# Kernel tuning notes

Hardware: AMD Instinct MI355X
Metric: run time of the kernel (lower is better)

Reference implementation:

```python
import jax, jax.numpy as jnp
import numpy as np

B, S = 1, 2048
H = 1024          # hidden_size
HQ = 16           # num_attention_heads
HKV = 1           # num_key_value_heads (MQA; required for torch matmul broadcast)
D = H // HQ       # head_dim = 64
FF = 4096         # intermediate_size
V = 32000         # vocab_size
L = 2             # num_hidden_layers
EPS = 1e-6


def setup_inputs() -> dict:
    key = jax.random.key(0)
    ks = jax.random.split(key, 12)
    s = 0.02
    return {
        "input_ids": jax.random.randint(ks[0], (B, S), 0, V, dtype=jnp.int32),
        "embed": jax.random.normal(ks[1], (V, H), jnp.float32) * s,
        "Wq": jax.random.normal(ks[2], (L, H, H), jnp.float32) * s,
        "Wk": jax.random.normal(ks[3], (L, HKV * D, H), jnp.float32) * s,
        "Wv": jax.random.normal(ks[4], (L, HKV * D, H), jnp.float32) * s,
        "Wo": jax.random.normal(ks[5], (L, H, H), jnp.float32) * s,
        "Wg": jax.random.normal(ks[6], (L, FF, H), jnp.float32) * s,
        "Wu": jax.random.normal(ks[7], (L, FF, H), jnp.float32) * s,
        "Wd": jax.random.normal(ks[8], (L, H, FF), jnp.float32) * s,
        "ln1": jnp.ones((L, H), jnp.float32),
        "ln2": jnp.ones((L, H), jnp.float32),
    }


def _rmsnorm(x, w):
    return x * jax.lax.rsqrt(jnp.mean(x * x, axis=-1, keepdims=True) + EPS) * w


def _rope(x):
    # x: [B, h, S, D]; module hardcodes base 10000 (ignores config theta)
    d = x.shape[-1]
    inv = 1.0 / (10000.0 ** (jnp.arange(0, d, 2, dtype=jnp.float32) / d))  # [d/2]
    freqs = jnp.arange(x.shape[2], dtype=jnp.float32)[:, None] * inv       # [S, d/2]
    cos, sin = jnp.cos(freqs), jnp.sin(freqs)
    x1, x2 = x[..., : d // 2], x[..., d // 2 :]
    return jnp.concatenate([x1 * cos - x2 * sin, x2 * cos + x1 * sin], axis=-1)


def _forward(input_ids, embed, Wq, Wk, Wv, Wo, Wg, Wu, Wd, ln1, ln2):
    x = embed[input_ids]  # [B, S, H]
    scale = 1.0 / jnp.sqrt(jnp.float32(D))
    for l in range(L):
        # --- attention ---
        h = _rmsnorm(x, ln1[l])
        q = (h @ Wq[l].T).reshape(B, S, HQ, D).transpose(0, 2, 1, 3)   # [B,HQ,S,D]
        k = (h @ Wk[l].T).reshape(B, S, HKV, D).transpose(0, 2, 1, 3)  # [B,1,S,D]
        v = (h @ Wv[l].T).reshape(B, S, HKV, D).transpose(0, 2, 1, 3)
        q, k = _rope(q), _rope(k)
        kk, vv = k[:, 0], v[:, 0]                                      # [B,S,D] (MQA broadcast)
        scores = jnp.einsum("bhqd,bkd->bhqk", q, kk) * scale           # [B,HQ,S,S] (no causal mask!)
        attn = jax.nn.softmax(scores, axis=-1)
        o = jnp.einsum("bhqk,bkd->bhqd", attn, vv)                     # [B,HQ,S,D]
        o = o.transpose(0, 2, 1, 3).reshape(B, S, H) @ Wo[l].T
        x = x + o
        # --- mlp (SwiGLU) ---
        h = _rmsnorm(x, ln2[l])
        x = x + (jax.nn.silu(h @ Wg[l].T) * (h @ Wu[l].T)) @ Wd[l].T
    return x


def reference(input_ids, embed, Wq, Wk, Wv, Wo, Wg, Wu, Wd, ln1, ln2):
    return _forward(input_ids, embed, Wq, Wk, Wv, Wo, Wg, Wu, Wd, ln1, ln2)
```

## Files before the change

kernel.cpp:

```cpp
#include <hip/hip_runtime.h>
#include <math.h>

#define S_LEN 2048
#define H_DIM 1024
#define NHQ 16
#define D_HEAD 64
#define FF_DIM 4096
#define NLAYER 2
#define EPSV 1e-6f
#define QKV_N 1152

typedef unsigned short ushortt;
typedef __attribute__((ext_vector_type(8))) short bf16x8;
typedef __attribute__((ext_vector_type(4))) short bf16x4;
typedef __attribute__((ext_vector_type(4))) float f32x4;
typedef __attribute__((ext_vector_type(16))) float f32x16;

__device__ __forceinline__ float bf2f(ushortt u) {
    union { float f; unsigned u; } c; c.u = ((unsigned)u) << 16; return c.f;
}
__device__ __forceinline__ ushortt f2bf(float f) {
    union { float f; unsigned u; } c; c.f = f;
    unsigned r = c.u + 0x7fff + ((c.u >> 16) & 1);
    return (ushortt)(r >> 16);
}
__device__ __forceinline__ unsigned cvtpk(float a, float b) {
    unsigned r;
    asm("v_cvt_pk_bf16_f32 %0, %1, %2" : "=v"(r) : "v"(a), "v"(b));
    return r;
}
__device__ __forceinline__ bf16x8 mk8(unsigned a, unsigned b, unsigned c, unsigned d) {
    union { unsigned u[4]; bf16x8 v; } t; t.u[0] = a; t.u[1] = b; t.u[2] = c; t.u[3] = d; return t.v;
}

__device__ __forceinline__ void gload_lds16(const ushortt* g, ushortt* l) {
    __builtin_amdgcn_global_load_lds(
        (const __attribute__((address_space(1))) unsigned int*)g,
        (__attribute__((address_space(3))) unsigned int*)l, 16, 0, 0);
}

__global__ __launch_bounds__(256) void f2b_k(const float* __restrict__ in,
                                             ushortt* __restrict__ out, long n) {
    long i8 = ((long)blockIdx.x * 256 + threadIdx.x) * 8;
    if (i8 >= n) return;
    f32x4 a = *(const f32x4*)&in[i8];
    f32x4 b = *(const f32x4*)&in[i8 + 4];
    bf16x8 o;
    #pragma unroll
    for (int j = 0; j < 4; j++) { o[j] = (short)f2bf(a[j]); o[4 + j] = (short)f2bf(b[j]); }
    *(bf16x8*)&out[i8] = o;
}

__global__ __launch_bounds__(256) void gather_k(const int* __restrict__ ids,
                                                const float* __restrict__ emb,
                                                float* __restrict__ x) {
    int row = blockIdx.x, tid = threadIdx.x;
    long id = ids[row];
    f32x4 e = *((const f32x4*)emb + id * (H_DIM / 4) + tid);
    *(f32x4*)&x[(long)row * H_DIM + tid * 4] = e;
}

__global__ __launch_bounds__(256) void rmsnorm_k(const float* __restrict__ x,
                                                 const float* __restrict__ w,
                                                 ushortt* __restrict__ out) {
    __shared__ float red[4];
    int row = blockIdx.x, tid = threadIdx.x;
    f32x4 v = *(const f32x4*)&x[(long)row * H_DIM + tid * 4];
    float ss = v[0]*v[0] + v[1]*v[1] + v[2]*v[2] + v[3]*v[3];
    #pragma unroll
    for (int off = 1; off < 64; off <<= 1) ss += __shfl_xor(ss, off, 64);
    if ((tid & 63) == 0) red[tid >> 6] = ss;
    __syncthreads();
    float tot = red[0] + red[1] + red[2] + red[3];
    float rs = rsqrtf(tot / (float)H_DIM + EPSV);
    f32x4 wv = *(const f32x4*)&w[tid * 4];
    #pragma unroll
    for (int j = 0; j < 4; j++)
        out[(long)row * H_DIM + tid * 4 + j] = f2bf(v[j] * rs * wv[j]);
}

template <int EPI>
__global__ __launch_bounds__(256) void gemm64(const ushortt* __restrict__ A,
                                              const ushortt* __restrict__ B,
                                              void* __restrict__ out,
                                              int M, int N, int K, int lda) {
    __shared__ ushortt As[2][64 * 64];
    __shared__ ushortt Bs[2][64 * 64];
    const int tid = threadIdx.x;
    const int lane = tid & 63;
    const int w = tid >> 6;
    const int wm = w >> 1, wn = w & 1;
    const int m0 = blockIdx.y * 64, n0 = blockIdx.x * 64;
    const int r15 = lane & 15, g = lane >> 4;

    const int sr = tid >> 3;
    const int scel = (tid & 7) * 8;
    const int swz = ((sr & 7) << 3);
    const int srcel = scel ^ swz;

    const ushortt* pa0 = &A[(long)(m0 + sr) * lda + srcel];
    const ushortt* pa1 = &A[(long)(m0 + 32 + sr) * lda + srcel];
    const ushortt* pb0 = &B[(long)(n0 + sr) * K + srcel];
    const ushortt* pb1 = &B[(long)(n0 + 32 + sr) * K + srcel];
    const int l0 = sr * 64 + scel, l1 = (32 + sr) * 64 + scel;

    f32x4 acc[2][2] = {};

#define STAGE(buf, t)                              \
    do {                                           \
        int kk_ = (t) * 64;                        \
        gload_lds16(pa0 + kk_, &As[buf][l0]);      \
        gload_lds16(pa1 + kk_, &As[buf][l1]);      \
        gload_lds16(pb0 + kk_, &Bs[buf][l0]);      \
        gload_lds16(pb1 + kk_, &Bs[buf][l1]);      \
    } while (0)

    STAGE(0, 0);
    asm volatile("s_waitcnt vmcnt(0)" : : : "memory");
    __builtin_amdgcn_s_barrier();

    const int NT = K / 64;
    int cur = 0;
    for (int t = 0; t < NT; ++t) {
        if (t + 1 < NT) STAGE(cur ^ 1, t + 1);

        bf16x8 a[2][2], b[2][2];
        #pragma unroll
        for (int mf = 0; mf < 2; mf++)
            #pragma unroll
            for (int ks = 0; ks < 2; ks++) {
                int row = wm * 32 + mf * 16 + r15;
                a[mf][ks] = *(bf16x8*)&As[cur][row * 64 + ((ks * 32 + g * 8) ^ ((row & 7) << 3))];
            }
        #pragma unroll
        for (int nf = 0; nf < 2; nf++)
            #pragma unroll
            for (int ks = 0; ks < 2; ks++) {
                int row = wn * 32 + nf * 16 + r15;
                b[nf][ks] = *(bf16x8*)&Bs[cur][row * 64 + ((ks * 32 + g * 8) ^ ((row & 7) << 3))];
            }
        #pragma unroll
        for (int ks = 0; ks < 2; ks++)
            #pragma unroll
            for (int mf = 0; mf < 2; mf++)
                #pragma unroll
                for (int nf = 0; nf < 2; nf++)
                    acc[mf][nf] = __builtin_amdgcn_mfma_f32_16x16x32_bf16(
                        a[mf][ks], b[nf][ks], acc[mf][nf], 0, 0, 0);

        asm volatile("s_waitcnt vmcnt(0)" : : : "memory");
        __builtin_amdgcn_s_barrier();
        cur ^= 1;
    }
#undef STAGE

    #pragma unroll
    for (int mf = 0; mf < 2; mf++)
        #pragma unroll
        for (int nf = 0; nf < 2; nf++)
            #pragma unroll
            for (int r = 0; r < 4; r++) {
                int row = m0 + wm * 32 + mf * 16 + g * 4 + r;
                int col = n0 + wn * 32 + nf * 16 + r15;
                float v = acc[mf][nf][r];
                if (EPI == 0) ((ushortt*)out)[(long)row * N + col] = f2bf(v);
                else ((float*)out)[(long)row * N + col] += v;
            }
}

__global__ __launch_bounds__(256) void rope_k(const ushortt* __restrict__ src,
                                              ushortt* __restrict__ dst,
                                              int nheads, int sstride, int dstride) {
    int idx = blockIdx.x * 256 + threadIdx.x;
    int total = S_LEN * nheads * 32;
    if (idx >= total) return;
    int i = idx & 31;
    int hd = (idx >> 5) % nheads;
    int s = idx / (32 * nheads);
    long sb = (long)s * sstride + hd * 64 + i;
    long db = (long)s * dstride + hd * 64 + i;
    float x1 = bf2f(src[sb]), x2 = bf2f(src[sb + 32]);
    float inv = expf(-((2.f * i) / 64.f) * 9.210340371976184f);
    float f = (float)s * inv;
    float sn, cs;
    sincosf(f, &sn, &cs);
    dst[db] = f2bf(x1 * cs - x2 * sn);
    dst[db + 32] = f2bf(x2 * cs + x1 * sn);
}

__global__ __launch_bounds__(256) void vtr_k(const ushortt* __restrict__ qkv,
                                             ushortt* __restrict__ vt) {
    __shared__ ushortt t[64][66];
    int s0 = blockIdx.x * 64;
    int grp = threadIdx.x >> 6, lane = threadIdx.x & 63;
    #pragma unroll
    for (int i = 0; i < 16; i++) {
        int r = grp * 16 + i;
        t[r][lane] = qkv[(long)(s0 + r) * QKV_N + NHQ * D_HEAD + D_HEAD + lane];
    }
    __syncthreads();
    #pragma unroll
    for (int i = 0; i < 16; i++) {
        int d = grp * 16 + i;
        vt[(long)d * S_LEN + s0 + lane] = t[lane][d];
    }
}

__device__ __forceinline__ void attn_body32(const bf16x8 ka[4], const bf16x8 va[4],
                                            const bf16x8 bq[4],
                                            f32x16& O0, f32x16& O1,
                                            float& lrun, int hb) {
    f32x16 s = {};
    #pragma unroll
    for (int ds = 0; ds < 4; ds++)
        s = __builtin_amdgcn_mfma_f32_32x32x16_bf16(ka[ds], bq[ds], s, 0, 0, 0);

    float p[16];
    float ps = 0.f;
    #pragma unroll
    for (int i = 0; i < 16; i++) {
        p[i] = __expf(s[i] * 0.125f);
        ps += p[i];
    }
    lrun += ps;

    unsigned w[8], x[8];
    #pragma unroll
    for (int t = 0; t < 8; t++) w[t] = cvtpk(p[2 * t], p[2 * t + 1]);
    #pragma unroll
    for (int t = 0; t < 8; t++) x[t] = __shfl_xor(w[t], 32, 64);
    bf16x8 B0 = hb ? mk8(x[2], x[3], w[2], w[3]) : mk8(w[0], w[1], x[0], x[1]);
    bf16x8 B1 = hb ? mk8(x[6], x[7], w[6], w[7]) : mk8(w[4], w[5], x[4], x[5]);

    O0 = __builtin_amdgcn_mfma_f32_32x32x16_bf16(va[0], B0, O0, 0, 0, 0);
    O0 = __builtin_amdgcn_mfma_f32_32x32x16_bf16(va[1], B1, O0, 0, 0, 0);
    O1 = __builtin_amdgcn_mfma_f32_32x32x16_bf16(va[2], B0, O1, 0, 0, 0);
    O1 = __builtin_amdgcn_mfma_f32_32x32x16_bf16(va[3], B1, O1, 0, 0, 0);
}

__global__ __launch_bounds__(256) void attn4_k(const ushortt* __restrict__ qkv,
                                               const ushortt* __restrict__ kb,
                                               const ushortt* __restrict__ vt,
                                               ushortt* __restrict__ o) {
    __shared__ float Olds[4][32 * 68];
    __shared__ float Llds[4][32];
    const int tid = threadIdx.x;
    const int w = tid >> 6;
    const int lane = tid & 63;
    const int l31 = lane & 31, hb = lane >> 5;
    const int h = blockIdx.y;
    const int q0 = blockIdx.x * 32;

    bf16x8 bq[4];
    #pragma unroll
    for (int ds = 0; ds < 4; ds++)
        bq[ds] = *(const bf16x8*)&qkv[(long)(q0 + l31) * QKV_N + h * D_HEAD + ds * 16 + hb * 8];

#define LOADKV(KA, VA, J0)                                                                \
    do {                                                                                  \
        _Pragma("unroll") for (int ds = 0; ds < 4; ds++)                                  \
            KA[ds] = *(const bf16x8*)&kb[(long)((J0) + l31) * D_HEAD + ds * 16 + hb * 8]; \
        _Pragma("unroll") for (int t = 0; t < 4; t++)                                     \
            VA[t] = *(const bf16x8*)&vt[(long)((t >> 1) * 32 + l31) * S_LEN + (J0) +      \
                                        (t & 1) * 16 + hb * 8];                           \
    } while (0)

    f32x16 O0 = {}, O1 = {};
    float lrun = 0.f;

    const int jbeg = w * (S_LEN / 4);
    const int jend = jbeg + (S_LEN / 4);

    bf16x8 kaA[4], vaA[4], kaB[4], vaB[4];
    LOADKV(kaA, vaA, jbeg);
    for (int j0 = jbeg; j0 < jend; j0 += 64) {
        LOADKV(kaB, vaB, j0 + 32);
        attn_body32(kaA, vaA, bq, O0, O1, lrun, hb);
        if (j0 + 64 < jend) LOADKV(kaA, vaA, j0 + 64);
        attn_body32(kaB, vaB, bq, O0, O1, lrun, hb);
    }
#undef LOADKV

    float ltot = lrun + __shfl_xor(lrun, 32, 64);
    #pragma unroll
    for (int r = 0; r < 16; r++) {
        int d = (r & 3) + 8 * (r >> 2) + 4 * hb;
        Olds[w][l31 * 68 + d] = O0[r];
        Olds[w][l31 * 68 + 32 + d] = O1[r];
    }
    if (hb == 0) Llds[w][l31] = ltot;
    __syncthreads();

    const int q = tid >> 3, d0 = (tid & 7) * 8;
    float denom = Llds[0][q] + Llds[1][q] + Llds[2][q] + Llds[3][q];
    float inv = 1.f / denom;
    float acc[8] = {};
    #pragma unroll
    for (int z = 0; z < 4; z++) {
        const float* p = &Olds[z][q * 68 + d0];
        f32x4 a = *(const f32x4*)p;
        f32x4 b = *(const f32x4*)(p + 4);
        #pragma unroll
        for (int j = 0; j < 4; j++) { acc[j] += a[j]; acc[4 + j] += b[j]; }
    }
    bf16x8 ov;
    #pragma unroll
    for (int j = 0; j < 8; j++) ov[j] = (short)f2bf(acc[j] * inv);
    *(bf16x8*)&o[(long)(q0 + q) * H_DIM + h * D_HEAD + d0] = ov;
}

__global__ __launch_bounds__(256) void silu_mul_k(const ushortt* __restrict__ gub,
                                                  ushortt* __restrict__ out, int n) {
    int idx = blockIdx.x * 256 + threadIdx.x;
    if (idx >= n) return;
    int row = idx >> 12;
    int c = idx & (FF_DIM - 1);
    float a = bf2f(gub[(long)row * (2 * FF_DIM) + c]);
    float b = bf2f(gub[(long)row * (2 * FF_DIM) + FF_DIM + c]);
    float r = (a / (1.f + __expf(-a))) * b;
    out[(long)row * (2 * FF_DIM) + c] = f2bf(r);
}

__global__ __launch_bounds__(256) void copy_out_k(const float* __restrict__ x,
                                                  float* __restrict__ out, int n4) {
    int idx = blockIdx.x * 256 + threadIdx.x;
    if (idx >= n4) return;
    *(f32x4*)&out[(long)idx * 4] = *(const f32x4*)&x[(long)idx * 4];
}

extern "C" void kernel_launch(void* const* d_in, const int* in_sizes, int n_in,
                              void* d_out, int out_size, void* d_ws, size_t ws_size,
                              hipStream_t stream) {
    const int* ids = (const int*)d_in[0];
    const float* emb = (const float*)d_in[1];
    const float* Wq = (const float*)d_in[2];
    const float* Wk = (const float*)d_in[3];
    const float* Wv = (const float*)d_in[4];
    const float* Wo = (const float*)d_in[5];
    const float* Wg = (const float*)d_in[6];
    const float* Wu = (const float*)d_in[7];
    const float* Wd = (const float*)d_in[8];
    const float* ln1 = (const float*)d_in[9];
    const float* ln2 = (const float*)d_in[10];

    char* ws = (char*)d_ws;
    float* x = (float*)ws;        ws += (size_t)S_LEN * H_DIM * 4;
    ushortt* qkv = (ushortt*)ws;  ws += (size_t)S_LEN * QKV_N * 2;
    ushortt* h = (ushortt*)ws;    ws += (size_t)S_LEN * H_DIM * 2;
    ushortt* kb = (ushortt*)ws;   ws += (size_t)S_LEN * D_HEAD * 2;
    ushortt* vt = (ushortt*)ws;   ws += (size_t)S_LEN * D_HEAD * 2;
    ushortt* ob = (ushortt*)ws;   ws += (size_t)S_LEN * H_DIM * 2;
    ushortt* gub = (ushortt*)ws;  ws += (size_t)S_LEN * 2 * FF_DIM * 2;
    ushortt* wt = (ushortt*)ws;   ws += (size_t)2 * FF_DIM * H_DIM * 2;

    auto conv = [&](const float* src, long n, long dstOff) {
        f2b_k<<<(int)((n / 8 + 255) / 256), 256, 0, stream>>>(src, wt + dstOff, n);
    };

    gather_k<<<S_LEN, 256, 0, stream>>>(ids, emb, x);

    for (int l = 0; l < NLAYER; l++) {
        rmsnorm_k<<<S_LEN, 256, 0, stream>>>(x, ln1 + (long)l * H_DIM, h);

        conv(Wq + (long)l * H_DIM * H_DIM, (long)H_DIM * H_DIM, 0);
        conv(Wk + (long)l * D_HEAD * H_DIM, (long)D_HEAD * H_DIM, (long)H_DIM * H_DIM);
        conv(Wv + (long)l * D_HEAD * H_DIM, (long)D_HEAD * H_DIM,
             (long)H_DIM * H_DIM + (long)D_HEAD * H_DIM);
        gemm64<0><<<dim3(QKV_N / 64, S_LEN / 64), 256, 0, stream>>>(
            h, wt, qkv, S_LEN, QKV_N, H_DIM, H_DIM);

        rope_k<<<(S_LEN * NHQ * 32 + 255) / 256, 256, 0, stream>>>(qkv, qkv, NHQ, QKV_N, QKV_N);
        rope_k<<<(S_LEN * 1 * 32 + 255) / 256, 256, 0, stream>>>(
            qkv + NHQ * D_HEAD, kb, 1, QKV_N, D_HEAD);
        vtr_k<<<S_LEN / 64, 256, 0, stream>>>(qkv, vt);

        attn4_k<<<dim3(S_LEN / 32, NHQ), 256, 0, stream>>>(qkv, kb, vt, ob);

        conv(Wo + (long)l * H_DIM * H_DIM, (long)H_DIM * H_DIM, 0);
        gemm64<1><<<dim3(H_DIM / 64, S_LEN / 64), 256, 0, stream>>>(ob, wt, x, S_LEN, H_DIM, H_DIM, H_DIM);

        rmsnorm_k<<<S_LEN, 256, 0, stream>>>(x, ln2 + (long)l * H_DIM, h);

        conv(Wg + (long)l * FF_DIM * H_DIM, (long)FF_DIM * H_DIM, 0);
        conv(Wu + (long)l * FF_DIM * H_DIM, (long)FF_DIM * H_DIM, (long)FF_DIM * H_DIM);
        gemm64<0><<<dim3(2 * FF_DIM / 64, S_LEN / 64), 256, 0, stream>>>(
            h, wt, gub, S_LEN, 2 * FF_DIM, H_DIM, H_DIM);
        silu_mul_k<<<(S_LEN * FF_DIM + 255) / 256, 256, 0, stream>>>(gub, gub, S_LEN * FF_DIM);
        conv(Wd + (long)l * H_DIM * FF_DIM, (long)H_DIM * FF_DIM, 0);
        gemm64<1><<<dim3(H_DIM / 64, S_LEN / 64), 256, 0, stream>>>(
            gub, wt, x, S_LEN, H_DIM, FF_DIM, 2 * FF_DIM);
    }

    copy_out_k<<<(out_size / 4 + 255) / 256, 256, 0, stream>>>(x, (float*)d_out, out_size / 4);
}
```

Before: 480.7 us.

## Fuse fp32-to-bf16 weight conversion into GEMM B-tile loads; use permlane32 swap in attention

Removes the separate f2b_k weight-conversion launches. Each GEMM now reads fp32 weights directly through registers, converts them to bf16 with cvt_pk and writes them to LDS, choosing among up to three weight tensors by column threshold. This saves the extra write and read of a bf16 weight copy and several launches, but every row block now re-reads fp32 weights (twice the bytes) and does the conversion redundantly. The B path also changes from async global_load_lds to register staging. Separately, attention replaces eight shfl_xor exchanges with four v_permlane32_swap instructions.

```diff
diff --git a/kernel.cpp b/kernel.cpp
--- a/kernel.cpp
+++ b/kernel.cpp
@@ -12,9 +12,9 @@
 
 typedef unsigned short ushortt;
 typedef __attribute__((ext_vector_type(8))) short bf16x8;
-typedef __attribute__((ext_vector_type(4))) short bf16x4;
 typedef __attribute__((ext_vector_type(4))) float f32x4;
 typedef __attribute__((ext_vector_type(16))) float f32x16;
+typedef __attribute__((ext_vector_type(4))) unsigned uint4v;
 
 __device__ __forceinline__ float bf2f(ushortt u) {
     union { float f; unsigned u; } c; c.u = ((unsigned)u) << 16; return c.f;
@@ -37,18 +37,6 @@
     __builtin_amdgcn_global_load_lds(
         (const __attribute__((address_space(1))) unsigned int*)g,
         (__attribute__((address_space(3))) unsigned int*)l, 16, 0, 0);
-}
-
-__global__ __launch_bounds__(256) void f2b_k(const float* __restrict__ in,
-                                             ushortt* __restrict__ out, long n) {
-    long i8 = ((long)blockIdx.x * 256 + threadIdx.x) * 8;
-    if (i8 >= n) return;
-    f32x4 a = *(const f32x4*)&in[i8];
-    f32x4 b = *(const f32x4*)&in[i8 + 4];
-    bf16x8 o;
-    #pragma unroll
-    for (int j = 0; j < 4; j++) { o[j] = (short)f2bf(a[j]); o[4 + j] = (short)f2bf(b[j]); }
-    *(bf16x8*)&out[i8] = o;
 }
 
 __global__ __launch_bounds__(256) void gather_k(const int* __restrict__ ids,
@@ -81,7 +69,10 @@
 
 template <int EPI>
 __global__ __launch_bounds__(256) void gemm64(const ushortt* __restrict__ A,
-                                              const ushortt* __restrict__ B,
+                                              const float* __restrict__ Bf0,
+                                              const float* __restrict__ Bf1,
+                                              const float* __restrict__ Bf2,
+                                              int thr1, int thr2,
                                               void* __restrict__ out,
                                               int M, int N, int K, int lda) {
     __shared__ ushortt As[2][64 * 64];
@@ -98,31 +89,53 @@
     const int swz = ((sr & 7) << 3);
     const int srcel = scel ^ swz;
 
+    const float* Bf; int nrel;
+    if (n0 >= thr2)      { Bf = Bf2; nrel = n0 - thr2; }
+    else if (n0 >= thr1) { Bf = Bf1; nrel = n0 - thr1; }
+    else                 { Bf = Bf0; nrel = n0; }
+
     const ushortt* pa0 = &A[(long)(m0 + sr) * lda + srcel];
     const ushortt* pa1 = &A[(long)(m0 + 32 + sr) * lda + srcel];
-    const ushortt* pb0 = &B[(long)(n0 + sr) * K + srcel];
-    const ushortt* pb1 = &B[(long)(n0 + 32 + sr) * K + srcel];
+    const float* pbf0 = &Bf[(long)(nrel + sr) * K + srcel];
+    const float* pbf1 = &Bf[(long)(nrel + 32 + sr) * K + srcel];
     const int l0 = sr * 64 + scel, l1 = (32 + sr) * 64 + scel;
 
     f32x4 acc[2][2] = {};
-
-#define STAGE(buf, t)                              \
+    f32x4 qa0, qa1, qb0, qb1;
+
+#define STAGE_A(buf, t)                            \
     do {                                           \
-        int kk_ = (t) * 64;                        \
+        long kk_ = (long)(t) * 64;                 \
         gload_lds16(pa0 + kk_, &As[buf][l0]);      \
         gload_lds16(pa1 + kk_, &As[buf][l1]);      \
-        gload_lds16(pb0 + kk_, &Bs[buf][l0]);      \
-        gload_lds16(pb1 + kk_, &Bs[buf][l1]);      \
     } while (0)
-
-    STAGE(0, 0);
-    asm volatile("s_waitcnt vmcnt(0)" : : : "memory");
+#define LOADB(t)                                   \
+    do {                                           \
+        long kk_ = (long)(t) * 64;                 \
+        qa0 = *(const f32x4*)(pbf0 + kk_);         \
+        qa1 = *(const f32x4*)(pbf0 + kk_ + 4);     \
+        qb0 = *(const f32x4*)(pbf1 + kk_);         \
+        qb1 = *(const f32x4*)(pbf1 + kk_ + 4);     \
+    } while (0)
+#define WRITEB(buf)                                                             \
+    do {                                                                        \
+        *(uint4v*)&Bs[buf][l0] = (uint4v){cvtpk(qa0[0], qa0[1]), cvtpk(qa0[2], qa0[3]), \
+                                          cvtpk(qa1[0], qa1[1]), cvtpk(qa1[2], qa1[3])}; \
+        *(uint4v*)&Bs[buf][l1] = (uint4v){cvtpk(qb0[0], qb0[1]), cvtpk(qb0[2], qb0[3]), \
+                                          cvtpk(qb1[0], qb1[1]), cvtpk(qb1[2], qb1[3])}; \
+    } while (0)
+
+    STAGE_A(0, 0);
+    LOADB(0);
+    WRITEB(0);
+    asm volatile("s_waitcnt vmcnt(0) lgkmcnt(0)" : : : "memory");
     __builtin_amdgcn_s_barrier();
 
     const int NT = K / 64;
     int cur = 0;
     for (int t = 0; t < NT; ++t) {
-        if (t + 1 < NT) STAGE(cur ^ 1, t + 1);
+        const int nb = cur ^ 1;
+        if (t + 1 < NT) { STAGE_A(nb, t + 1); LOADB(t + 1); }
 
         bf16x8 a[2][2], b[2][2];
         #pragma unroll
@@ -148,11 +161,14 @@
                     acc[mf][nf] = __builtin_amdgcn_mfma_f32_16x16x32_bf16(
                         a[mf][ks], b[nf][ks], acc[mf][nf], 0, 0, 0);
 
-        asm volatile("s_waitcnt vmcnt(0)" : : : "memory");
+        if (t + 1 < NT) WRITEB(nb);
+        asm volatile("s_waitcnt vmcnt(0) lgkmcnt(0)" : : : "memory");
         __builtin_amdgcn_s_barrier();
         cur ^= 1;
     }
-#undef STAGE
+#undef STAGE_A
+#undef LOADB
+#undef WRITEB
 
     #pragma unroll
     for (int mf = 0; mf < 2; mf++)
@@ -209,7 +225,7 @@
 __device__ __forceinline__ void attn_body32(const bf16x8 ka[4], const bf16x8 va[4],
                                             const bf16x8 bq[4],
                                             f32x16& O0, f32x16& O1,
-                                            float& lrun, int hb) {
+                                            float& lrun) {
     f32x16 s = {};
     #pragma unroll
     for (int ds = 0; ds < 4; ds++)
@@ -224,13 +240,16 @@
     }
     lrun += ps;
 
-    unsigned w[8], x[8];
-    #pragma unroll
-    for (int t = 0; t < 8; t++) w[t] = cvtpk(p[2 * t], p[2 * t + 1]);
-    #pragma unroll
-    for (int t = 0; t < 8; t++) x[t] = __shfl_xor(w[t], 32, 64);
-    bf16x8 B0 = hb ? mk8(x[2], x[3], w[2], w[3]) : mk8(w[0], w[1], x[0], x[1]);
-    bf16x8 B1 = hb ? mk8(x[6], x[7], w[6], w[7]) : mk8(w[4], w[5], x[4], x[5]);
+    unsigned w0 = cvtpk(p[0], p[1]),  w1 = cvtpk(p[2], p[3]);
+    unsigned w2 = cvtpk(p[4], p[5]),  w3 = cvtpk(p[6], p[7]);
+    unsigned w4 = cvtpk(p[8], p[9]),  w5 = cvtpk(p[10], p[11]);
+    unsigned w6 = cvtpk(p[12], p[13]), w7 = cvtpk(p[14], p[15]);
+    asm volatile("v_permlane32_swap_b32 %0, %1" : "+v"(w0), "+v"(w2));
+    asm volatile("v_permlane32_swap_b32 %0, %1" : "+v"(w1), "+v"(w3));
+    asm volatile("v_permlane32_swap_b32 %0, %1" : "+v"(w4), "+v"(w6));
+    asm volatile("v_permlane32_swap_b32 %0, %1" : "+v"(w5), "+v"(w7));
+    bf16x8 B0 = mk8(w0, w1, w2, w3);
+    bf16x8 B1 = mk8(w4, w5, w6, w7);
 
     O0 = __builtin_amdgcn_mfma_f32_32x32x16_bf16(va[0], B0, O0, 0, 0, 0);
     O0 = __builtin_amdgcn_mfma_f32_32x32x16_bf16(va[1], B1, O0, 0, 0, 0);
@@ -275,9 +294,9 @@
     LOADKV(kaA, vaA, jbeg);
     for (int j0 = jbeg; j0 < jend; j0 += 64) {
         LOADKV(kaB, vaB, j0 + 32);
-        attn_body32(kaA, vaA, bq, O0, O1, lrun, hb);
+        attn_body32(kaA, vaA, bq, O0, O1, lrun);
         if (j0 + 64 < jend) LOADKV(kaA, vaA, j0 + 64);
-        attn_body32(kaB, vaB, bq, O0, O1, lrun, hb);
+        attn_body32(kaB, vaB, bq, O0, O1, lrun);
     }
 #undef LOADKV
 
@@ -351,23 +370,24 @@
     ushortt* vt = (ushortt*)ws;   ws += (size_t)S_LEN * D_HEAD * 2;
     ushortt* ob = (ushortt*)ws;   ws += (size_t)S_LEN * H_DIM * 2;
     ushortt* gub = (ushortt*)ws;  ws += (size_t)S_LEN * 2 * FF_DIM * 2;
-    ushortt* wt = (ushortt*)ws;   ws += (size_t)2 * FF_DIM * H_DIM * 2;
-
-    auto conv = [&](const float* src, long n, long dstOff) {
-        f2b_k<<<(int)((n / 8 + 255) / 256), 256, 0, stream>>>(src, wt + dstOff, n);
-    };
+
+    const int BIG = 1 << 30;
 
     gather_k<<<S_LEN, 256, 0, stream>>>(ids, emb, x);
 
     for (int l = 0; l < NLAYER; l++) {
+        const float* Wq_l = Wq + (long)l * H_DIM * H_DIM;
+        const float* Wk_l = Wk + (long)l * D_HEAD * H_DIM;
+        const float* Wv_l = Wv + (long)l * D_HEAD * H_DIM;
+        const float* Wo_l = Wo + (long)l * H_DIM * H_DIM;
+        const float* Wg_l = Wg + (long)l * FF_DIM * H_DIM;
+        const float* Wu_l = Wu + (long)l * FF_DIM * H_DIM;
+        const float* Wd_l = Wd + (long)l * H_DIM * FF_DIM;
+
         rmsnorm_k<<<S_LEN, 256, 0, stream>>>(x, ln1 + (long)l * H_DIM, h);
 
-        conv(Wq + (long)l * H_DIM * H_DIM, (long)H_DIM * H_DIM, 0);
-        conv(Wk + (long)l * D_HEAD * H_DIM, (long)D_HEAD * H_DIM, (long)H_DIM * H_DIM);
-        conv(Wv + (long)l * D_HEAD * H_DIM, (long)D_HEAD * H_DIM,
-             (long)H_DIM * H_DIM + (long)D_HEAD * H_DIM);
         gemm64<0><<<dim3(QKV_N / 64, S_LEN / 64), 256, 0, stream>>>(
-            h, wt, qkv, S_LEN, QKV_N, H_DIM, H_DIM);
+            h, Wq_l, Wk_l, Wv_l, H_DIM, H_DIM + D_HEAD, qkv, S_LEN, QKV_N, H_DIM, H_DIM);
 
         rope_k<<<(S_LEN * NHQ * 32 + 255) / 256, 256, 0, stream>>>(qkv, qkv, NHQ, QKV_N, QKV_N);
         rope_k<<<(S_LEN * 1 * 32 + 255) / 256, 256, 0, stream>>>(
@@ -376,19 +396,16 @@
 
         attn4_k<<<dim3(S_LEN / 32, NHQ), 256, 0, stream>>>(qkv, kb, vt, ob);
 
-        conv(Wo + (long)l * H_DIM * H_DIM, (long)H_DIM * H_DIM, 0);
-        gemm64<1><<<dim3(H_DIM / 64, S_LEN / 64), 256, 0, stream>>>(ob, wt, x, S_LEN, H_DIM, H_DIM, H_DIM);
+        gemm64<1><<<dim3(H_DIM / 64, S_LEN / 64), 256, 0, stream>>>(
+            ob, Wo_l, Wo_l, Wo_l, BIG, BIG, x, S_LEN, H_DIM, H_DIM, H_DIM);
 
         rmsnorm_k<<<S_LEN, 256, 0, stream>>>(x, ln2 + (long)l * H_DIM, h);
 
-        conv(Wg + (long)l * FF_DIM * H_DIM, (long)FF_DIM * H_DIM, 0);
-        conv(Wu + (long)l * FF_DIM * H_DIM, (long)FF_DIM * H_DIM, (long)FF_DIM * H_DIM);
         gemm64<0><<<dim3(2 * FF_DIM / 64, S_LEN / 64), 256, 0, stream>>>(
-            h, wt, gub, S_LEN, 2 * FF_DIM, H_DIM, H_DIM);
+            h, Wg_l, Wu_l, Wu_l, FF_DIM, BIG, gub, S_LEN, 2 * FF_DIM, H_DIM, H_DIM);
         silu_mul_k<<<(S_LEN * FF_DIM + 255) / 256, 256, 0, stream>>>(gub, gub, S_LEN * FF_DIM);
-        conv(Wd + (long)l * H_DIM * FF_DIM, (long)H_DIM * FF_DIM, 0);
         gemm64<1><<<dim3(H_DIM / 64, S_LEN / 64), 256, 0, stream>>>(
-            gub, wt, x, S_LEN, H_DIM, FF_DIM, 2 * FF_DIM);
+            gub, Wd_l, Wd_l, Wd_l, BIG, BIG, x, S_LEN, H_DIM, FF_DIM, 2 * FF_DIM);
     }
 
     copy_out_k<<<(out_size / 4 + 255) / 256, 256, 0, stream>>>(x, (float*)d_out, out_size / 4);
```

New measurement: 505.4 us. 5.1% more time.
